# Kernel tuning notes

Measured on AMD Instinct MI355X. Metric: run time of the kernel, lower is better.

The kernel has to match this reference:

```python
import jax, jax.numpy as jnp
import numpy as np

K, N = 64, 4096

def setup_inputs() -> dict:
    key = jax.random.key(0)
    k1, k2 = jax.random.split(key)
    zs = jax.random.uniform(k1, (K, N), dtype=jnp.float32)        # K candidate schedules
    X = jax.random.uniform(k2, (N, N), dtype=jnp.float32)         # channel gain matrix
    var_noise = jnp.asarray(1.0, dtype=jnp.float32)
    return {"zs": zs, "X": X, "var_noise": var_noise}

def reference(zs, X, var_noise):
    # Original per-sample math: all_info[i,j] = z[j]*X[i,j]
    #   numerators   = diag(all_info) = z * diag(X)
    #   denominators = row_sum(all_info) - numerators = X @ z - numerators
    # Batched over K zs: one GEMM instead of K O(n^2) elementwise products.
    row_sums = jnp.einsum('kn,in->ki', zs, X)       # [K, N] = (X @ z_k)_i
    numerators = zs * jnp.diagonal(X)[None, :]      # [K, N]
    denominators = row_sums - numerators            # [K, N]
    per_sample = -jnp.sum(numerators / (var_noise + denominators), axis=1)  # [K]
    return jnp.sum(per_sample) / zs.shape[0]
```

## Files before the change

kernel.cpp:

```cpp
#include <hip/hip_runtime.h>

#define K_DIM 64
#define N_DIM 4096

typedef float  f4   __attribute__((ext_vector_type(4)));
typedef short  s8v  __attribute__((ext_vector_type(8)));

static __device__ __forceinline__ unsigned short f2bf(float f) {
    unsigned int u = __builtin_bit_cast(unsigned int, f);
    u = (u + 0x7fffu + ((u >> 16) & 1u)) >> 16;
    return (unsigned short)u;
}

__global__ void init_kernel(const float* __restrict__ X, float* __restrict__ rs,
                            float* __restrict__ diag, float* __restrict__ out) {
    int gid = blockIdx.x * 256 + threadIdx.x;
    if (gid < K_DIM * N_DIM) rs[gid] = 0.f;
    if (gid < N_DIM) diag[gid] = X[gid * (N_DIM + 1)];
    if (gid == 0) *out = 0.f;
}

__global__ __launch_bounds__(256, 2) void gemm_rs_kernel(
    const float* __restrict__ zs, const float* __restrict__ X,
    float* __restrict__ rs) {
    __shared__ s8v zs_l[16 * 64];
    __shared__ s8v x_l [32 * 64];

    const int tid  = threadIdx.x;
    const int lane = tid & 63;
    const int w    = tid >> 6;
    const int i0   = blockIdx.y * 128;
    const int nb0  = blockIdx.x * 256;

    f4 acc[8] = {};

    for (int sc = 0; sc < 2; ++sc) {
        const int nsub = nb0 + sc * 128;

        #pragma unroll
        for (int it = 0; it < 4; ++it) {
            int p = tid + it * 256;
            int k = p >> 4, q = p & 15;
            const float* g = zs + k * N_DIM + nsub + q * 8;
            f4 f0 = *(const f4*)g;
            f4 f1 = *(const f4*)(g + 4);
            s8v h;
            h[0] = (short)f2bf(f0[0]); h[1] = (short)f2bf(f0[1]);
            h[2] = (short)f2bf(f0[2]); h[3] = (short)f2bf(f0[3]);
            h[4] = (short)f2bf(f1[0]); h[5] = (short)f2bf(f1[1]);
            h[6] = (short)f2bf(f1[2]); h[7] = (short)f2bf(f1[3]);
            int kb = k >> 4, nb = q >> 2;
            int dl = ((kb * 4 + nb) << 6) | (k & 15) | ((q & 3) << 4);
            zs_l[dl] = h;
        }
        #pragma unroll
        for (int it = 0; it < 8; ++it) {
            int p = tid + it * 256;
            int il = p >> 4, q = p & 15;
            const float* g = X + (i0 + il) * N_DIM + nsub + q * 8;
            f4 f0 = *(const f4*)g;
            f4 f1 = *(const f4*)(g + 4);
            s8v h;
            h[0] = (short)f2bf(f0[0]); h[1] = (short)f2bf(f0[1]);
            h[2] = (short)f2bf(f0[2]); h[3] = (short)f2bf(f0[3]);
            h[4] = (short)f2bf(f1[0]); h[5] = (short)f2bf(f1[1]);
            h[6] = (short)f2bf(f1[2]); h[7] = (short)f2bf(f1[3]);
            int ibl = il >> 4, nb = q >> 2;
            int dl = ((ibl * 4 + nb) << 6) | (il & 15) | ((q & 3) << 4);
            x_l[dl] = h;
        }
        __syncthreads();

        #pragma unroll
        for (int nb = 0; nb < 4; ++nb) {
            s8v a = zs_l[((w * 4 + nb) << 6) | lane];
            #pragma unroll
            for (int ibl = 0; ibl < 8; ++ibl) {
                s8v b = x_l[((ibl * 4 + nb) << 6) | lane];
                acc[ibl] = __builtin_amdgcn_mfma_f32_16x16x32_bf16(a, b, acc[ibl], 0, 0, 0);
            }
        }
        __syncthreads();
    }

    const int krow = w * 16 + ((lane >> 4) << 2);
    const int icol = i0 + (lane & 15);
    #pragma unroll
    for (int ibl = 0; ibl < 8; ++ibl) {
        #pragma unroll
        for (int r = 0; r < 4; ++r) {
            atomicAdd(&rs[(krow + r) * N_DIM + icol + ibl * 16], acc[ibl][r]);
        }
    }
}

__global__ void epilogue_kernel(const float* __restrict__ rs,
                                const float* __restrict__ zs,
                                const float* __restrict__ diag,
                                const float* __restrict__ varp,
                                float* __restrict__ out) {
    const float var = *varp;
    const int tid = threadIdx.x;
    float sum = 0.f;
    for (int idx = blockIdx.x * 256 + tid; idx < K_DIM * N_DIM; idx += gridDim.x * 256) {
        int i = idx & (N_DIM - 1);
        float z   = zs[idx];
        float num = z * diag[i];
        float den = rs[idx] - num;
        sum += num / (var + den);
    }
    #pragma unroll
    for (int off = 32; off >= 1; off >>= 1) sum += __shfl_down(sum, off);
    __shared__ float wsum[4];
    if ((tid & 63) == 0) wsum[tid >> 6] = sum;
    __syncthreads();
    if (tid == 0)
        atomicAdd(out, -(wsum[0] + wsum[1] + wsum[2] + wsum[3]) * (1.0f / 64.0f));
}

extern "C" void kernel_launch(void* const* d_in, const int* in_sizes, int n_in,
                              void* d_out, int out_size, void* d_ws, size_t ws_size,
                              hipStream_t stream) {
    const float* zs   = (const float*)d_in[0];
    const float* X    = (const float*)d_in[1];
    const float* varp = (const float*)d_in[2];
    float* out  = (float*)d_out;
    float* rs   = (float*)d_ws;
    float* diag = rs + K_DIM * N_DIM;

    hipLaunchKernelGGL(init_kernel, dim3(1024), dim3(256), 0, stream, X, rs, diag, out);
    hipLaunchKernelGGL(gemm_rs_kernel, dim3(16, 32), dim3(256), 0, stream, zs, X, rs);
    hipLaunchKernelGGL(epilogue_kernel, dim3(256), dim3(256), 0, stream, rs, zs, diag, varp, out);
}
```

Baseline: 121.8 us.

## Fuse GEMM and epilogue into one full-K kernel with register-prefetched double buffering

Replaces the split-N GEMM, which used atomics into a row-sum workspace, plus the separate init and epilogue kernels with one fused kernel. Each block owns 16 output rows, loops over all of N with register prefetch and double-buffered LDS, then computes the ratio terms and the reduction straight from its accumulators. This removes millions of global atomics, the workspace round trip and two launches. In exchange every block rereads the whole zs matrix from cache, and occupancy is low: 256 blocks of 4 waves with a serial 32-step loop.

```diff
diff --git a/kernel.cpp b/kernel.cpp
--- a/kernel.cpp
+++ b/kernel.cpp
@@ -1,118 +1,104 @@
 #include <hip/hip_runtime.h>
 
-#define K_DIM 64
 #define N_DIM 4096
 
-typedef float  f4   __attribute__((ext_vector_type(4)));
-typedef short  s8v  __attribute__((ext_vector_type(8)));
+typedef float f4  __attribute__((ext_vector_type(4)));
+typedef short s8v __attribute__((ext_vector_type(8)));
 
 static __device__ __forceinline__ unsigned short f2bf(float f) {
     unsigned int u = __builtin_bit_cast(unsigned int, f);
     u = (u + 0x7fffu + ((u >> 16) & 1u)) >> 16;
     return (unsigned short)u;
 }
-
-__global__ void init_kernel(const float* __restrict__ X, float* __restrict__ rs,
-                            float* __restrict__ diag, float* __restrict__ out) {
-    int gid = blockIdx.x * 256 + threadIdx.x;
-    if (gid < K_DIM * N_DIM) rs[gid] = 0.f;
-    if (gid < N_DIM) diag[gid] = X[gid * (N_DIM + 1)];
-    if (gid == 0) *out = 0.f;
+static __device__ __forceinline__ s8v pack8(f4 a, f4 b) {
+    s8v h;
+    h[0] = (short)f2bf(a[0]); h[1] = (short)f2bf(a[1]);
+    h[2] = (short)f2bf(a[2]); h[3] = (short)f2bf(a[3]);
+    h[4] = (short)f2bf(b[0]); h[5] = (short)f2bf(b[1]);
+    h[6] = (short)f2bf(b[2]); h[7] = (short)f2bf(b[3]);
+    return h;
 }
 
-__global__ __launch_bounds__(256, 2) void gemm_rs_kernel(
+__global__ void zero_out_kernel(float* __restrict__ out) {
+    if (threadIdx.x == 0 && blockIdx.x == 0) out[0] = 0.f;
+}
+
+__global__ __launch_bounds__(256, 1) void fused_kernel(
     const float* __restrict__ zs, const float* __restrict__ X,
-    float* __restrict__ rs) {
-    __shared__ s8v zs_l[16 * 64];
-    __shared__ s8v x_l [32 * 64];
+    const float* __restrict__ varp, float* __restrict__ out) {
+    __shared__ s8v zs_l[2][1024];
+    __shared__ s8v x_l [2][256];
 
     const int tid  = threadIdx.x;
     const int lane = tid & 63;
     const int w    = tid >> 6;
-    const int i0   = blockIdx.y * 128;
-    const int nb0  = blockIdx.x * 256;
+    const int i0   = blockIdx.x * 16;
 
-    f4 acc[8] = {};
+    f4 acc = {0.f, 0.f, 0.f, 0.f};
+    f4 rz[8], rx[2];
 
-    for (int sc = 0; sc < 2; ++sc) {
-        const int nsub = nb0 + sc * 128;
+    #pragma unroll
+    for (int it = 0; it < 4; ++it) {
+        int idx = it * 256 + tid;
+        const f4* g = (const f4*)(zs + ((idx >> 8) * 16 + (idx & 15)) * N_DIM
+                                     + ((idx >> 4) & 15) * 8);
+        rz[2 * it] = g[0]; rz[2 * it + 1] = g[1];
+    }
+    {
+        const f4* gx = (const f4*)(X + (size_t)(i0 + (tid & 15)) * N_DIM
+                                      + ((tid >> 4) & 15) * 8);
+        rx[0] = gx[0]; rx[1] = gx[1];
+    }
+    #pragma unroll
+    for (int it = 0; it < 4; ++it)
+        zs_l[0][it * 256 + tid] = pack8(rz[2 * it], rz[2 * it + 1]);
+    x_l[0][tid] = pack8(rx[0], rx[1]);
 
-        #pragma unroll
-        for (int it = 0; it < 4; ++it) {
-            int p = tid + it * 256;
-            int k = p >> 4, q = p & 15;
-            const float* g = zs + k * N_DIM + nsub + q * 8;
-            f4 f0 = *(const f4*)g;
-            f4 f1 = *(const f4*)(g + 4);
-            s8v h;
-            h[0] = (short)f2bf(f0[0]); h[1] = (short)f2bf(f0[1]);
-            h[2] = (short)f2bf(f0[2]); h[3] = (short)f2bf(f0[3]);
-            h[4] = (short)f2bf(f1[0]); h[5] = (short)f2bf(f1[1]);
-            h[6] = (short)f2bf(f1[2]); h[7] = (short)f2bf(f1[3]);
-            int kb = k >> 4, nb = q >> 2;
-            int dl = ((kb * 4 + nb) << 6) | (k & 15) | ((q & 3) << 4);
-            zs_l[dl] = h;
-        }
-        #pragma unroll
-        for (int it = 0; it < 8; ++it) {
-            int p = tid + it * 256;
-            int il = p >> 4, q = p & 15;
-            const float* g = X + (i0 + il) * N_DIM + nsub + q * 8;
-            f4 f0 = *(const f4*)g;
-            f4 f1 = *(const f4*)(g + 4);
-            s8v h;
-            h[0] = (short)f2bf(f0[0]); h[1] = (short)f2bf(f0[1]);
-            h[2] = (short)f2bf(f0[2]); h[3] = (short)f2bf(f0[3]);
-            h[4] = (short)f2bf(f1[0]); h[5] = (short)f2bf(f1[1]);
-            h[6] = (short)f2bf(f1[2]); h[7] = (short)f2bf(f1[3]);
-            int ibl = il >> 4, nb = q >> 2;
-            int dl = ((ibl * 4 + nb) << 6) | (il & 15) | ((q & 3) << 4);
-            x_l[dl] = h;
+    for (int c = 0; c < 32; ++c) {
+        const int cur = c & 1, nxt = cur ^ 1;
+        if (c < 31) {
+            const int n0 = (c + 1) * 128;
+            #pragma unroll
+            for (int it = 0; it < 4; ++it) {
+                int idx = it * 256 + tid;
+                const f4* g = (const f4*)(zs + ((idx >> 8) * 16 + (idx & 15)) * N_DIM
+                                             + n0 + ((idx >> 4) & 15) * 8);
+                rz[2 * it] = g[0]; rz[2 * it + 1] = g[1];
+            }
+            const f4* gx = (const f4*)(X + (size_t)(i0 + (tid & 15)) * N_DIM
+                                          + n0 + ((tid >> 4) & 15) * 8);
+            rx[0] = gx[0]; rx[1] = gx[1];
         }
         __syncthreads();
-
         #pragma unroll
-        for (int nb = 0; nb < 4; ++nb) {
-            s8v a = zs_l[((w * 4 + nb) << 6) | lane];
+        for (int s = 0; s < 4; ++s) {
+            s8v a = zs_l[cur][(w * 4 + s) * 64 + lane];
+            s8v b = x_l[cur][s * 64 + lane];
+            acc = __builtin_amdgcn_mfma_f32_16x16x32_bf16(a, b, acc, 0, 0, 0);
+        }
+        if (c < 31) {
             #pragma unroll
-            for (int ibl = 0; ibl < 8; ++ibl) {
-                s8v b = x_l[((ibl * 4 + nb) << 6) | lane];
-                acc[ibl] = __builtin_amdgcn_mfma_f32_16x16x32_bf16(a, b, acc[ibl], 0, 0, 0);
-            }
+            for (int it = 0; it < 4; ++it)
+                zs_l[nxt][it * 256 + tid] = pack8(rz[2 * it], rz[2 * it + 1]);
+            x_l[nxt][tid] = pack8(rx[0], rx[1]);
         }
-        __syncthreads();
     }
 
-    const int krow = w * 16 + ((lane >> 4) << 2);
-    const int icol = i0 + (lane & 15);
+    const int   i_g  = i0 + (lane & 15);
+    const float diag = X[(size_t)i_g * N_DIM + i_g];
+    const float var  = varp[0];
+    float lsum = 0.f;
     #pragma unroll
-    for (int ibl = 0; ibl < 8; ++ibl) {
-        #pragma unroll
-        for (int r = 0; r < 4; ++r) {
-            atomicAdd(&rs[(krow + r) * N_DIM + icol + ibl * 16], acc[ibl][r]);
-        }
-    }
-}
-
-__global__ void epilogue_kernel(const float* __restrict__ rs,
-                                const float* __restrict__ zs,
-                                const float* __restrict__ diag,
-                                const float* __restrict__ varp,
-                                float* __restrict__ out) {
-    const float var = *varp;
-    const int tid = threadIdx.x;
-    float sum = 0.f;
-    for (int idx = blockIdx.x * 256 + tid; idx < K_DIM * N_DIM; idx += gridDim.x * 256) {
-        int i = idx & (N_DIM - 1);
-        float z   = zs[idx];
-        float num = z * diag[i];
-        float den = rs[idx] - num;
-        sum += num / (var + den);
+    for (int r = 0; r < 4; ++r) {
+        int   k   = 16 * w + ((lane >> 4) << 2) + r;
+        float num = zs[k * N_DIM + i_g] * diag;
+        float den = acc[r] - num;
+        lsum += num / (var + den);
     }
     #pragma unroll
-    for (int off = 32; off >= 1; off >>= 1) sum += __shfl_down(sum, off);
+    for (int off = 32; off >= 1; off >>= 1) lsum += __shfl_down(lsum, off);
     __shared__ float wsum[4];
-    if ((tid & 63) == 0) wsum[tid >> 6] = sum;
+    if (lane == 0) wsum[w] = lsum;
     __syncthreads();
     if (tid == 0)
         atomicAdd(out, -(wsum[0] + wsum[1] + wsum[2] + wsum[3]) * (1.0f / 64.0f));
@@ -124,11 +110,8 @@
     const float* zs   = (const float*)d_in[0];
     const float* X    = (const float*)d_in[1];
     const float* varp = (const float*)d_in[2];
-    float* out  = (float*)d_out;
-    float* rs   = (float*)d_ws;
-    float* diag = rs + K_DIM * N_DIM;
+    float* out = (float*)d_out;
 
-    hipLaunchKernelGGL(init_kernel, dim3(1024), dim3(256), 0, stream, X, rs, diag, out);
-    hipLaunchKernelGGL(gemm_rs_kernel, dim3(16, 32), dim3(256), 0, stream, zs, X, rs);
-    hipLaunchKernelGGL(epilogue_kernel, dim3(256), dim3(256), 0, stream, rs, zs, diag, varp, out);
+    hipLaunchKernelGGL(zero_out_kernel, dim3(1), dim3(64), 0, stream, out);
+    hipLaunchKernelGGL(fused_kernel, dim3(256), dim3(256), 0, stream, zs, X, varp, out);
 }
```

New measurement: 130.3 us. +7.0%, slower.
